# Optimization experiments

Measured on AMD Instinct MI355X. Metric: run time of the kernel, lower is better.

Reference implementation:

```python
import jax, jax.numpy as jnp
import numpy as np

H = 4      # hidden_size
L = 5      # num_layers
IN = 1     # input_size
B = 1024   # batch
T = 2048   # seq_len


def setup_inputs() -> dict:
    key = jax.random.key(0)
    ks = jax.random.split(key, 6)
    s = 1.0 / np.sqrt(H)  # PyTorch LSTM init: U(-1/sqrt(H), 1/sqrt(H))
    u = lambda k, shape: jax.random.uniform(k, shape, jnp.float32, -s, s)
    return {
        "x": jax.random.normal(ks[0], (B, T, IN), jnp.float32),
        "w_ih0": u(ks[1], (4 * H, IN)),          # layer 0 input weights
        "w_ih_rest": u(ks[2], (L - 1, 4 * H, H)),  # layers 1..L-1 input weights
        "w_hh": u(ks[3], (L, 4 * H, H)),
        "b_ih": u(ks[4], (L, 4 * H)),
        "b_hh": u(ks[5], (L, 4 * H)),
    }


def _lstm_layer(seq, w_ih, w_hh, b_ih, b_hh):
    # seq: [T, B, in] -> outputs [T, B, H], final hidden [B, H]
    # Precompute input contributions for all timesteps (one big GEMM).
    gx = jnp.einsum('tbi,gi->tbg', seq, w_ih) + b_ih + b_hh  # [T, B, 4H]
    h0 = jnp.zeros((seq.shape[1], H), seq.dtype)
    c0 = h0

    def step(carry, g_t):
        h, c = carry
        g = g_t + h @ w_hh.T                      # [B, 4H]
        i, f, gc, o = jnp.split(g, 4, axis=-1)    # PyTorch gate order i,f,g,o
        i = jax.nn.sigmoid(i)
        f = jax.nn.sigmoid(f)
        o = jax.nn.sigmoid(o)
        c = f * c + i * jnp.tanh(gc)
        h = o * jnp.tanh(c)
        return (h, c), h

    (hT, _), out = jax.lax.scan(step, (h0, c0), gx)
    return out, hT


def reference(x, w_ih0, w_ih_rest, w_hh, b_ih, b_hh):
    seq = jnp.transpose(x, (1, 0, 2))  # batch_first -> time-major [T, B, IN]
    out, hT = _lstm_layer(seq, w_ih0, w_hh[0], b_ih[0], b_hh[0])
    for l in range(L - 1):  # fixed small layer count; structural loop is fine
        out, hT = _lstm_layer(out, w_ih_rest[l], w_hh[l + 1], b_ih[l + 1], b_hh[l + 1])
    # final hidden state of the last (top) layer == rnn_hidden_states[-1]
    return hT  # [B, H]
```

## Files before the change

### kernel.cpp

```cpp
#include <hip/hip_runtime.h>
#include <stdint.h>


#define T_LEN   2048
#define NLAYER  5
#define CHUNK   16
#define NCHUNK  (T_LEN / CHUNK)
#define NPHASE  (NCHUNK + NLAYER - 1)

template <int CTRL>
__device__ __forceinline__ float dppmov(float x) {
  int v = __builtin_amdgcn_mov_dpp(__float_as_int(x), CTRL, 0xF, 0xF, true);
  return __int_as_float(v);
}

__global__ void __launch_bounds__(64 * NLAYER, 1) lstm_pipe(
    const float* __restrict__ x,
    const float* __restrict__ w_ih0,
    const float* __restrict__ w_ih_rest,
    const float* __restrict__ w_hh,
    const float* __restrict__ b_ih,
    const float* __restrict__ b_hh,
    float* __restrict__ out)
{
  const int tid  = threadIdx.x;
  const int l    = tid >> 6;
  const int lane = tid & 63;
  const int q    = lane & 15;
  const int el   = lane >> 4;
  const int e    = blockIdx.x * 4 + el;
  const int gt   = q & 3;
  const int j    = q >> 2;
  const int r    = gt * 4 + j;

  const float LOG2E = 1.4426950408889634f;
  const float s = (gt == 2) ? (-2.0f * LOG2E) : (-LOG2E);

  float whh[4];
  float wih[4] = {0.f, 0.f, 0.f, 0.f};
  #pragma unroll
  for (int m = 0; m < 4; ++m) {
    const int k = (j - m) & 3;
    whh[m] = w_hh[l * 64 + r * 4 + k] * s;
  }
  if (l > 0) {
    #pragma unroll
    for (int m = 0; m < 4; ++m) {
      const int k = (j - m) & 3;
      wih[m] = w_ih_rest[(l - 1) * 64 + r * 4 + k] * s;
    }
  }
  float wx = 0.f;
  if (l == 0) wx = w_ih0[r] * s;
  const float bias = (b_ih[l * 16 + r] + b_hh[l * 16 + r]) * s;

  float hr0 = 0.f, hr1 = 0.f, hr2 = 0.f, hr3 = 0.f;
  float c = 0.f;

  __shared__ float buf[NLAYER - 1][2][CHUNK][4][16];

  float gx[CHUNK];

  for (int p = 0; p < NPHASE; ++p) {
    const int n = p - l;
    if (n >= 0 && n < NCHUNK) {
      const int par = n & 1;
      const int t0  = n * CHUNK;

      if (l == 0) {
        #pragma unroll
        for (int tc = 0; tc < CHUNK; ++tc)
          gx[tc] = fmaf(wx, x[e * T_LEN + t0 + tc], bias);
      } else {
        #pragma unroll
        for (int tc = 0; tc < CHUNK; ++tc) {
          const float a0 = buf[l - 1][par][tc][el][q];
          const float a1 = dppmov<0x124>(a0);
          const float a2 = dppmov<0x128>(a0);
          const float a3 = dppmov<0x12C>(a0);
          float acc = bias;
          acc = fmaf(wih[0], a0, acc);
          acc = fmaf(wih[1], a1, acc);
          acc = fmaf(wih[2], a2, acc);
          acc = fmaf(wih[3], a3, acc);
          gx[tc] = acc;
        }
      }

      #pragma unroll
      for (int tc = 0; tc < CHUNK; ++tc) {
        float t01 = fmaf(whh[0], hr0, gx[tc]);
        t01 = fmaf(whh[1], hr1, t01);
        float t23 = whh[2] * hr2;
        t23 = fmaf(whh[3], hr3, t23);
        float acc = t01 + t23;

        acc = fminf(acc, 126.f);
        const float E = __builtin_amdgcn_exp2f(acc);
        const float A = 1.f + E;
        const float R = __builtin_amdgcn_rcpf(A);
        const float act = (gt == 2) ? (2.f - A) * R : R;

        const float iv = dppmov<0x00>(act);
        const float fv = dppmov<0x55>(act);
        const float gv = dppmov<0xAA>(act);
        const float ov = dppmov<0xFF>(act);

        c = fmaf(fv, c, iv * gv);
        const float ct = fminf(c * (-2.f * LOG2E), 126.f);
        const float E2 = __builtin_amdgcn_exp2f(ct);
        const float A2 = 1.f + E2;
        const float R2 = __builtin_amdgcn_rcpf(A2);
        const float h  = ov * ((2.f - A2) * R2);

        hr0 = h;
        hr1 = dppmov<0x124>(h);
        hr2 = dppmov<0x128>(h);
        hr3 = dppmov<0x12C>(h);

        if (l < NLAYER - 1) buf[l][par][tc][el][q] = h;
      }

      if (l == NLAYER - 1 && n == NCHUNK - 1 && gt == 0) out[e * 4 + j] = hr0;
    }
    __syncthreads();
  }
}

extern "C" void kernel_launch(void* const* d_in, const int* in_sizes, int n_in,
                              void* d_out, int out_size, void* d_ws, size_t ws_size,
                              hipStream_t stream) {
  const float* x     = (const float*)d_in[0];
  const float* wih0  = (const float*)d_in[1];
  const float* wrest = (const float*)d_in[2];
  const float* whh   = (const float*)d_in[3];
  const float* bih   = (const float*)d_in[4];
  const float* bhh   = (const float*)d_in[5];
  float* out = (float*)d_out;

  dim3 grid(256);
  dim3 block(64 * NLAYER);
  lstm_pipe<<<grid, block, 0, stream>>>(x, wih0, wrest, whh, bih, bhh, out);
}
```

Baseline: 345.3 us.

## Double chunk size, prefetch x, trim activation math, split store path

```diff
diff --git a/kernel.cpp b/kernel.cpp
--- a/kernel.cpp
+++ b/kernel.cpp
@@ -4,7 +4,7 @@
 
 #define T_LEN   2048
 #define NLAYER  5
-#define CHUNK   16
+#define CHUNK   32
 #define NCHUNK  (T_LEN / CHUNK)
 #define NPHASE  (NCHUNK + NLAYER - 1)
 
@@ -12,6 +12,47 @@
 __device__ __forceinline__ float dppmov(float x) {
   int v = __builtin_amdgcn_mov_dpp(__float_as_int(x), CTRL, 0xF, 0xF, true);
   return __int_as_float(v);
+}
+
+template <bool STORE>
+__device__ __forceinline__ void lstm_step(
+    float gxv, const float* whh, float k1, float k0,
+    float& hr0, float& hr1, float& hr2, float& hr3, float& c,
+    float* __restrict__ slot)
+{
+  const float LOG2E = 1.4426950408889634f;
+
+  float t01 = fmaf(whh[0], hr0, gxv);
+  t01 = fmaf(whh[1], hr1, t01);
+  float t23 = whh[2] * hr2;
+  t23 = fmaf(whh[3], hr3, t23);
+  const float acc = t01 + t23;
+
+  const float E = __builtin_amdgcn_exp2f(acc);
+  const float A = 1.f + E;
+  const float R = __builtin_amdgcn_rcpf(A);
+  const float act = fmaf(k1, R, k0);
+
+  const float iv = dppmov<0x00>(act);
+  const float fv = dppmov<0x55>(act);
+  const float gv = dppmov<0xAA>(act);
+  const float ov = dppmov<0xFF>(act);
+  const float ov2 = ov + ov;
+  const float ovm = -ov;
+
+  c = fmaf(fv, c, iv * gv);
+  const float ct = c * (-2.0f * LOG2E);
+  const float E2 = __builtin_amdgcn_exp2f(ct);
+  const float A2 = 1.f + E2;
+  const float R2 = __builtin_amdgcn_rcpf(A2);
+  const float h  = fmaf(ov2, R2, ovm);
+
+  hr0 = h;
+  hr1 = dppmov<0x124>(h);
+  hr2 = dppmov<0x128>(h);
+  hr3 = dppmov<0x12C>(h);
+
+  if (STORE) *slot = h;
 }
 
 __global__ void __launch_bounds__(64 * NLAYER, 1) lstm_pipe(
@@ -34,7 +75,9 @@
   const int r    = gt * 4 + j;
 
   const float LOG2E = 1.4426950408889634f;
-  const float s = (gt == 2) ? (-2.0f * LOG2E) : (-LOG2E);
+  const float s  = (gt == 2) ? (-2.0f * LOG2E) : (-LOG2E);
+  const float k1 = (gt == 2) ? 2.0f : 1.0f;
+  const float k0 = (gt == 2) ? -1.0f : 0.0f;
 
   float whh[4];
   float wih[4] = {0.f, 0.f, 0.f, 0.f};
@@ -60,17 +103,27 @@
   __shared__ float buf[NLAYER - 1][2][CHUNK][4][16];
 
   float gx[CHUNK];
+  float xcur[CHUNK];
+
+  if (l == 0) {
+    #pragma unroll
+    for (int tc = 0; tc < CHUNK; ++tc) xcur[tc] = x[e * T_LEN + tc];
+  }
 
   for (int p = 0; p < NPHASE; ++p) {
     const int n = p - l;
     if (n >= 0 && n < NCHUNK) {
       const int par = n & 1;
-      const int t0  = n * CHUNK;
 
       if (l == 0) {
         #pragma unroll
         for (int tc = 0; tc < CHUNK; ++tc)
-          gx[tc] = fmaf(wx, x[e * T_LEN + t0 + tc], bias);
+          gx[tc] = fmaf(wx, xcur[tc], bias);
+        if (n + 1 < NCHUNK) {
+          #pragma unroll
+          for (int tc = 0; tc < CHUNK; ++tc)
+            xcur[tc] = x[e * T_LEN + (n + 1) * CHUNK + tc];
+        }
       } else {
         #pragma unroll
         for (int tc = 0; tc < CHUNK; ++tc) {
@@ -78,48 +131,28 @@
           const float a1 = dppmov<0x124>(a0);
           const float a2 = dppmov<0x128>(a0);
           const float a3 = dppmov<0x12C>(a0);
-          float acc = bias;
-          acc = fmaf(wih[0], a0, acc);
+          float acc = fmaf(wih[0], a0, bias);
           acc = fmaf(wih[1], a1, acc);
-          acc = fmaf(wih[2], a2, acc);
-          acc = fmaf(wih[3], a3, acc);
-          gx[tc] = acc;
+          float acc2 = wih[2] * a2;
+          acc2 = fmaf(wih[3], a3, acc2);
+          gx[tc] = acc + acc2;
         }
       }
 
-      #pragma unroll
-      for (int tc = 0; tc < CHUNK; ++tc) {
-        float t01 = fmaf(whh[0], hr0, gx[tc]);
-        t01 = fmaf(whh[1], hr1, t01);
-        float t23 = whh[2] * hr2;
-        t23 = fmaf(whh[3], hr3, t23);
-        float acc = t01 + t23;
-
-        acc = fminf(acc, 126.f);
-        const float E = __builtin_amdgcn_exp2f(acc);
-        const float A = 1.f + E;
-        const float R = __builtin_amdgcn_rcpf(A);
-        const float act = (gt == 2) ? (2.f - A) * R : R;
-
-        const float iv = dppmov<0x00>(act);
-        const float fv = dppmov<0x55>(act);
-        const float gv = dppmov<0xAA>(act);
-        const float ov = dppmov<0xFF>(act);
-
-        c = fmaf(fv, c, iv * gv);
-        const float ct = fminf(c * (-2.f * LOG2E), 126.f);
-        const float E2 = __builtin_amdgcn_exp2f(ct);
-        const float A2 = 1.f + E2;
-        const float R2 = __builtin_amdgcn_rcpf(A2);
-        const float h  = ov * ((2.f - A2) * R2);
-
-        hr0 = h;
-        hr1 = dppmov<0x124>(h);
-        hr2 = dppmov<0x128>(h);
-        hr3 = dppmov<0x12C>(h);
-
-        if (l < NLAYER - 1) buf[l][par][tc][el][q] = h;
+      __builtin_amdgcn_s_setprio(1);
+      if (l < NLAYER - 1) {
+        float* slotbase = &buf[l][par][0][el][q];
+        #pragma unroll
+        for (int tc = 0; tc < CHUNK; ++tc)
+          lstm_step<true>(gx[tc], whh, k1, k0, hr0, hr1, hr2, hr3, c,
+                          slotbase + tc * 64);
+      } else {
+        #pragma unroll
+        for (int tc = 0; tc < CHUNK; ++tc)
+          lstm_step<false>(gx[tc], whh, k1, k0, hr0, hr1, hr2, hr3, c,
+                           nullptr);
       }
+      __builtin_amdgcn_s_setprio(0);
 
       if (l == NLAYER - 1 && n == NCHUNK - 1 && gt == 0) out[e * 4 + j] = hr0;
     }
```

New measurement: 299.9 us. -13.1%, faster.
